# Optimization experiments

Hardware: AMD Instinct MI355X
Metric: run time of the kernel (lower is better)

## Reference

```python
import jax, jax.numpy as jnp
import numpy as np

B, S, DIN, DOUT = 4, 2048, 4096, 11008

def setup_inputs() -> dict:
    key = jax.random.key(0)
    k1, k2, k3 = jax.random.split(key, 3)
    x = jax.random.normal(k1, (B, S, DIN), dtype=jnp.float32)
    # int8 weight stored as int32 for portability; values in int8 range
    weight = jax.random.randint(k2, (DOUT, DIN), -127, 128, dtype=jnp.int32)
    scales = jax.random.uniform(k3, (DOUT,), dtype=jnp.float32) * 0.02 + 0.001
    return {"x": x, "weight": weight, "scales": scales}

def reference(x, weight, scales):
    # F.linear(input, weight.to(input.dtype)) * scales
    w = weight.astype(x.dtype)                      # [DOUT, DIN]
    out = jnp.einsum('bsi,oi->bso', x, w)           # [B, S, DOUT]
    return out * scales                             # per-out-channel scale
```

## Files before the change

### kernel.cpp

```cpp
#include <hip/hip_runtime.h>
#include <hip/hip_bf16.h>

#define M_DIM 8192
#define N_DIM 11008
#define K_DIM 4096

typedef __attribute__((ext_vector_type(8))) short bf16x8;
typedef __attribute__((ext_vector_type(4))) float f32x4;
typedef __attribute__((ext_vector_type(4))) int i32x4;

__device__ __forceinline__ short f2bf(float f) {
    __hip_bfloat16 h = __float2bfloat16(f);
    short s;
    __builtin_memcpy(&s, &h, sizeof(s));
    return s;
}

__device__ __forceinline__ void gload_lds16(const void* g, void* l) {
    __builtin_amdgcn_global_load_lds(
        (const __attribute__((address_space(1))) unsigned int*)g,
        (__attribute__((address_space(3))) unsigned int*)l, 16, 0, 0);
}

#define MFMAI8(A, Bv, C) __builtin_amdgcn_mfma_i32_16x16x64_i8((A), (Bv), (C), 0, 0, 0)
#define MFMA16(A, Bv, C) __builtin_amdgcn_mfma_f32_16x16x32_bf16((A), (Bv), (C), 0, 0, 0)


__global__ __launch_bounds__(256)
void quant_x_i8(const float* __restrict__ X, char* __restrict__ Xq,
                float* __restrict__ RS) {
    const int row  = blockIdx.x * 4 + (threadIdx.x >> 6);
    const int lane = threadIdx.x & 63;
    const float* xr = X + (size_t)row * K_DIM;

    float4 v[16];
    float am = 0.0f;
    #pragma unroll
    for (int c = 0; c < 16; ++c) {
        v[c] = *reinterpret_cast<const float4*>(xr + c * 256 + lane * 4);
        am = fmaxf(am, fmaxf(fmaxf(fabsf(v[c].x), fabsf(v[c].y)),
                             fmaxf(fabsf(v[c].z), fabsf(v[c].w))));
    }
    #pragma unroll
    for (int off = 1; off < 64; off <<= 1)
        am = fmaxf(am, __shfl_xor(am, off));

    const float inv = 127.0f / am;
    int* xq32 = reinterpret_cast<int*>(Xq + (size_t)row * K_DIM);
    #pragma unroll
    for (int c = 0; c < 16; ++c) {
        int c0 = __float2int_rn(v[c].x * inv);
        int c1 = __float2int_rn(v[c].y * inv);
        int c2 = __float2int_rn(v[c].z * inv);
        int c3 = __float2int_rn(v[c].w * inv);
        xq32[c * 64 + lane] = (c0 & 255) | ((c1 & 255) << 8) |
                              ((c2 & 255) << 16) | (c3 << 24);
    }
    if (lane == 0) RS[row] = am / 127.0f;
}


__global__ __launch_bounds__(256)
void cvt_w_i8(const int* __restrict__ W, char* __restrict__ Wq, int n16) {
    int i = blockIdx.x * blockDim.x + threadIdx.x;
    const int stride = gridDim.x * blockDim.x;
    for (; i < n16; i += stride) {
        const int4* p = reinterpret_cast<const int4*>(W + (size_t)i * 16);
        int4 a = p[0], b = p[1], c = p[2], d = p[3];
        int4 o;
        o.x = (a.x & 255) | ((a.y & 255) << 8) | ((a.z & 255) << 16) | (a.w << 24);
        o.y = (b.x & 255) | ((b.y & 255) << 8) | ((b.z & 255) << 16) | (b.w << 24);
        o.z = (c.x & 255) | ((c.y & 255) << 8) | ((c.z & 255) << 16) | (c.w << 24);
        o.w = (d.x & 255) | ((d.y & 255) << 8) | ((d.z & 255) << 16) | (d.w << 24);
        *reinterpret_cast<int4*>(Wq + (size_t)i * 16) = o;
    }
}


#define ST_A(T, DSTB) do { \
    const char* s_ = gA + (size_t)(T) * 128; \
    char* d_ = (DSTB) + aw; \
    gload_lds16(s_,                         d_); \
    gload_lds16(s_ + (size_t)64  * K_DIM,   d_ + 8192); \
    gload_lds16(s_ + (size_t)128 * K_DIM,   d_ + 16384); \
    gload_lds16(s_ + (size_t)192 * K_DIM,   d_ + 24576); \
} while (0)

#define ST_B(T, DSTB) do { \
    const char* s_ = gB + (size_t)(T) * 128; \
    char* d_ = (DSTB) + aw; \
    gload_lds16(s_,                         d_); \
    gload_lds16(s_ + (size_t)64  * K_DIM,   d_ + 8192); \
    gload_lds16(s_ + (size_t)128 * K_DIM,   d_ + 16384); \
    gload_lds16(s_ + (size_t)192 * K_DIM,   d_ + 24576); \
} while (0)

__global__ __launch_bounds__(512, 2)
void gemm_i8_nb(const char* __restrict__ Xq, const char* __restrict__ Wq,
                const float* __restrict__ RS, const float* __restrict__ SC,
                float* __restrict__ Out)
{
    __shared__ __attribute__((aligned(16))) char smem[163840];
    char* const As = smem;
    char* const Bs = smem + 65536;

    const int tid  = threadIdx.x;
    const int lane = tid & 63;
    const int w    = tid >> 6;
    const int wr   = w >> 2;
    const int wc   = w & 3;

    const int wg  = blockIdx.x;
    const int swz = (wg & 7) * 172 + (wg >> 3);
    const int by  = swz / 43;
    const int bx  = swz - by * 43;
    const int brow = by * 256;
    const int bcol = bx * 256;

    const int lr = lane >> 3;
    const int lc = (lane & 7) ^ lr;
    const char* gA = Xq + (size_t)(brow + w * 8 + lr) * K_DIM + (lc << 4);
    const char* gB = Wq + (size_t)(bcol + w * 8 + lr) * K_DIM + (lc << 4);
    const int aw = w * 1024;

    const int fa  = (wr * 128 + (lane & 15)) * 128;
    const int fb  = (wc * 64  + (lane & 15)) * 128;
    const int cs0 = (((lane >> 4) + 0) ^ (lane & 7)) * 16;
    const int cs1 = (((lane >> 4) + 4) ^ (lane & 7)) * 16;

    i32x4 acc[4][4] = {};
    i32x4 acc2[4][4] = {};

    char* Ac = As;            char* An = As + 32768;
    char* Bc = Bs;  char* B1 = Bs + 32768;  char* B2 = Bs + 65536;

    ST_B(0, Bc); ST_A(0, Ac);
    ST_B(1, B1);
    asm volatile("s_waitcnt vmcnt(4)" ::: "memory");
    __builtin_amdgcn_s_barrier();

    for (int t = 0; t < 32; ++t) {
        i32x4 a_[8][2], b_[4][2];
        #pragma unroll
        for (int m = 0; m < 4; ++m) {
            a_[m][0] = *(const i32x4*)(Ac + fa + m * 2048 + cs0);
            a_[m][1] = *(const i32x4*)(Ac + fa + m * 2048 + cs1);
        }
        #pragma unroll
        for (int n = 0; n < 4; ++n) {
            b_[n][0] = *(const i32x4*)(Bc + fb + n * 2048 + cs0);
            b_[n][1] = *(const i32x4*)(Bc + fb + n * 2048 + cs1);
        }
        if (t < 31) ST_A(t + 1, An);
        if (t < 30) ST_B(t + 2, B2);
        #pragma unroll
        for (int m = 0; m < 4; ++m) {
            a_[m + 4][0] = *(const i32x4*)(Ac + fa + (m + 4) * 2048 + cs0);
            a_[m + 4][1] = *(const i32x4*)(Ac + fa + (m + 4) * 2048 + cs1);
        }
        __builtin_amdgcn_s_setprio(1);
        #pragma unroll
        for (int m = 0; m < 4; ++m)
            #pragma unroll
            for (int n = 0; n < 4; ++n) {
                acc[m][n] = MFMAI8(a_[m][0], b_[n][0], acc[m][n]);
                acc[m][n] = MFMAI8(a_[m][1], b_[n][1], acc[m][n]);
            }
        #pragma unroll
        for (int m = 0; m < 4; ++m)
            #pragma unroll
            for (int n = 0; n < 4; ++n) {
                acc2[m][n] = MFMAI8(a_[m + 4][0], b_[n][0], acc2[m][n]);
                acc2[m][n] = MFMAI8(a_[m + 4][1], b_[n][1], acc2[m][n]);
            }
        __builtin_amdgcn_s_setprio(0);
        if (t < 31) {
            if (t < 30) asm volatile("s_waitcnt vmcnt(4)" ::: "memory");
            else        asm volatile("s_waitcnt vmcnt(0)" ::: "memory");
            __builtin_amdgcn_s_barrier();
        }
        char* tA = Ac; Ac = An; An = tA;
        char* tB = Bc; Bc = B1; B1 = B2; B2 = tB;
    }

    const int orow0 = brow + wr * 128 + ((lane >> 4) << 2);
    const int ocol0 = bcol + wc * 64 + (lane & 15);
    f32x4 rsv[8];
    #pragma unroll
    for (int m = 0; m < 8; ++m)
        rsv[m] = *reinterpret_cast<const f32x4*>(&RS[orow0 + m * 16]);
    #pragma unroll
    for (int n = 0; n < 4; ++n) {
        const float sc = SC[ocol0 + n * 16];
        #pragma unroll
        for (int m = 0; m < 4; ++m)
            #pragma unroll
            for (int j = 0; j < 4; ++j) {
                __builtin_nontemporal_store(
                    (float)acc[m][n][j] * (rsv[m][j] * sc),
                    &Out[(size_t)(orow0 + m * 16 + j) * N_DIM + (ocol0 + n * 16)]);
                __builtin_nontemporal_store(
                    (float)acc2[m][n][j] * (rsv[m + 4][j] * sc),
                    &Out[(size_t)(orow0 + (m + 4) * 16 + j) * N_DIM + (ocol0 + n * 16)]);
            }
    }
}


__global__ __launch_bounds__(256, 2)
void wo_int8_gemm_fused(const float* __restrict__ X, const int* __restrict__ W,
                        const float* __restrict__ SC, float* __restrict__ Out)
{
    __shared__ short Asf[128 * 64];
    __shared__ short Bsf[128 * 64];

    const int tid  = threadIdx.x;
    const int lane = tid & 63;
    const int wid  = tid >> 6;
    const int wrf  = wid >> 1;
    const int wcf  = wid & 1;
    const int brow = blockIdx.y * 128;
    const int bcol = blockIdx.x * 128;
    const int srow = tid >> 3;
    const int scol = (tid & 7) << 3;
    const int arow   = wrf * 64 + (lane & 15);
    const int brow_f = wcf * 64 + (lane & 15);
    const int koff   = (lane >> 4) << 3;

    f32x4 acc[4][4] = {};

    for (int k0 = 0; k0 < K_DIM; k0 += 64) {
        __syncthreads();
        #pragma unroll
        for (int p = 0; p < 4; ++p) {
            const int r = p * 32 + srow;
            const float4* xs = reinterpret_cast<const float4*>(
                X + (size_t)(brow + r) * K_DIM + (k0 + scol));
            float4 a0 = xs[0], a1 = xs[1];
            bf16x8 v;
            v[0] = f2bf(a0.x); v[1] = f2bf(a0.y); v[2] = f2bf(a0.z); v[3] = f2bf(a0.w);
            v[4] = f2bf(a1.x); v[5] = f2bf(a1.y); v[6] = f2bf(a1.z); v[7] = f2bf(a1.w);
            *reinterpret_cast<bf16x8*>(&Asf[(r * 64 + scol) ^ ((r & 7) << 3)]) = v;
        }
        #pragma unroll
        for (int p = 0; p < 4; ++p) {
            const int r = p * 32 + srow;
            const int4* ws = reinterpret_cast<const int4*>(
                W + (size_t)(bcol + r) * K_DIM + (k0 + scol));
            int4 b0 = ws[0], b1 = ws[1];
            bf16x8 v;
            v[0] = f2bf((float)b0.x); v[1] = f2bf((float)b0.y);
            v[2] = f2bf((float)b0.z); v[3] = f2bf((float)b0.w);
            v[4] = f2bf((float)b1.x); v[5] = f2bf((float)b1.y);
            v[6] = f2bf((float)b1.z); v[7] = f2bf((float)b1.w);
            *reinterpret_cast<bf16x8*>(&Bsf[(r * 64 + scol) ^ ((r & 7) << 3)]) = v;
        }
        __syncthreads();
        #pragma unroll
        for (int ks = 0; ks < 2; ++ks) {
            const int kb = ks * 32 + koff;
            bf16x8 af[4], bfr[4];
            #pragma unroll
            for (int m = 0; m < 4; ++m) {
                const int r = arow + m * 16;
                af[m] = *reinterpret_cast<const bf16x8*>(&Asf[(r * 64 + kb) ^ ((r & 7) << 3)]);
            }
            #pragma unroll
            for (int n = 0; n < 4; ++n) {
                const int r = brow_f + n * 16;
                bfr[n] = *reinterpret_cast<const bf16x8*>(&Bsf[(r * 64 + kb) ^ ((r & 7) << 3)]);
            }
            #pragma unroll
            for (int m = 0; m < 4; ++m)
                #pragma unroll
                for (int n = 0; n < 4; ++n)
                    acc[m][n] = MFMA16(af[m], bfr[n], acc[m][n]);
        }
    }

    const int orow0 = brow + wrf * 64 + ((lane >> 4) << 2);
    const int ocol0 = bcol + wcf * 64 + (lane & 15);
    #pragma unroll
    for (int n = 0; n < 4; ++n) {
        const float sc = SC[ocol0 + n * 16];
        #pragma unroll
        for (int m = 0; m < 4; ++m)
            #pragma unroll
            for (int j = 0; j < 4; ++j)
                Out[(size_t)(orow0 + m * 16 + j) * N_DIM + (ocol0 + n * 16)]
                    = acc[m][n][j] * sc;
    }
}

extern "C" void kernel_launch(void* const* d_in, const int* in_sizes, int n_in,
                              void* d_out, int out_size, void* d_ws, size_t ws_size,
                              hipStream_t stream) {
    const float* X  = (const float*)d_in[0];
    const int*   W  = (const int*)d_in[1];
    const float* SC = (const float*)d_in[2];
    float* Out = (float*)d_out;

    const size_t xq_bytes = (size_t)M_DIM * K_DIM;
    const size_t wq_bytes = (size_t)N_DIM * K_DIM;
    const size_t rs_bytes = (size_t)M_DIM * sizeof(float);
    if (ws_size >= xq_bytes + wq_bytes + rs_bytes) {
        char*  Xq = (char*)d_ws;
        char*  Wq = (char*)d_ws + xq_bytes;
        float* RS = (float*)((char*)d_ws + xq_bytes + wq_bytes);
        quant_x_i8<<<M_DIM / 4, 256, 0, stream>>>(X, Xq, RS);
        cvt_w_i8<<<2048, 256, 0, stream>>>(W, Wq, (int)((size_t)N_DIM * K_DIM / 16));
        gemm_i8_nb<<<(M_DIM / 256) * (N_DIM / 256), 512, 0, stream>>>(Xq, Wq, RS, SC, Out);
    } else {
        dim3 grid(N_DIM / 128, M_DIM / 128);
        wo_int8_gemm_fused<<<grid, 256, 0, stream>>>(X, W, SC, Out);
    }
}
```

Before: 453.9 us.

## Load GEMM fragments directly from global memory into registers, dropping LDS staging

Removes the shared-memory tiles, the async global-to-LDS copies, the multi-buffer rotation and the per-iteration barriers from the int8 GEMM. Each wave now loads its A and B MFMA fragments straight from global memory into registers every K step. This cuts LDS traffic and synchronisation, but gives up the data reuse across waves and the prefetch overlap. Global and L2 traffic goes up, and load latency is exposed with no software pipelining.

```diff
diff --git a/kernel.cpp b/kernel.cpp
--- a/kernel.cpp
+++ b/kernel.cpp
@@ -14,12 +14,6 @@
     short s;
     __builtin_memcpy(&s, &h, sizeof(s));
     return s;
-}
-
-__device__ __forceinline__ void gload_lds16(const void* g, void* l) {
-    __builtin_amdgcn_global_load_lds(
-        (const __attribute__((address_space(1))) unsigned int*)g,
-        (__attribute__((address_space(3))) unsigned int*)l, 16, 0, 0);
 }
 
 #define MFMAI8(A, Bv, C) __builtin_amdgcn_mfma_i32_16x16x64_i8((A), (Bv), (C), 0, 0, 0)
@@ -77,33 +71,11 @@
 }
 
 
-#define ST_A(T, DSTB) do { \
-    const char* s_ = gA + (size_t)(T) * 128; \
-    char* d_ = (DSTB) + aw; \
-    gload_lds16(s_,                         d_); \
-    gload_lds16(s_ + (size_t)64  * K_DIM,   d_ + 8192); \
-    gload_lds16(s_ + (size_t)128 * K_DIM,   d_ + 16384); \
-    gload_lds16(s_ + (size_t)192 * K_DIM,   d_ + 24576); \
-} while (0)
-
-#define ST_B(T, DSTB) do { \
-    const char* s_ = gB + (size_t)(T) * 128; \
-    char* d_ = (DSTB) + aw; \
-    gload_lds16(s_,                         d_); \
-    gload_lds16(s_ + (size_t)64  * K_DIM,   d_ + 8192); \
-    gload_lds16(s_ + (size_t)128 * K_DIM,   d_ + 16384); \
-    gload_lds16(s_ + (size_t)192 * K_DIM,   d_ + 24576); \
-} while (0)
-
 __global__ __launch_bounds__(512, 2)
-void gemm_i8_nb(const char* __restrict__ Xq, const char* __restrict__ Wq,
-                const float* __restrict__ RS, const float* __restrict__ SC,
-                float* __restrict__ Out)
+void gemm_i8_reg(const char* __restrict__ Xq, const char* __restrict__ Wq,
+                 const float* __restrict__ RS, const float* __restrict__ SC,
+                 float* __restrict__ Out)
 {
-    __shared__ __attribute__((aligned(16))) char smem[163840];
-    char* const As = smem;
-    char* const Bs = smem + 65536;
-
     const int tid  = threadIdx.x;
     const int lane = tid & 63;
     const int w    = tid >> 6;
@@ -117,70 +89,48 @@
     const int brow = by * 256;
     const int bcol = bx * 256;
 
-    const int lr = lane >> 3;
-    const int lc = (lane & 7) ^ lr;
-    const char* gA = Xq + (size_t)(brow + w * 8 + lr) * K_DIM + (lc << 4);
-    const char* gB = Wq + (size_t)(bcol + w * 8 + lr) * K_DIM + (lc << 4);
-    const int aw = w * 1024;
-
-    const int fa  = (wr * 128 + (lane & 15)) * 128;
-    const int fb  = (wc * 64  + (lane & 15)) * 128;
-    const int cs0 = (((lane >> 4) + 0) ^ (lane & 7)) * 16;
-    const int cs1 = (((lane >> 4) + 4) ^ (lane & 7)) * 16;
+    const char* pA = Xq + (size_t)(brow + wr * 128 + (lane & 15)) * K_DIM
+                        + ((lane >> 4) << 4);
+    const char* pB = Wq + (size_t)(bcol + wc * 64 + (lane & 15)) * K_DIM
+                        + ((lane >> 4) << 4);
 
     i32x4 acc[4][4] = {};
     i32x4 acc2[4][4] = {};
 
-    char* Ac = As;            char* An = As + 32768;
-    char* Bc = Bs;  char* B1 = Bs + 32768;  char* B2 = Bs + 65536;
-
-    ST_B(0, Bc); ST_A(0, Ac);
-    ST_B(1, B1);
-    asm volatile("s_waitcnt vmcnt(4)" ::: "memory");
-    __builtin_amdgcn_s_barrier();
-
     for (int t = 0; t < 32; ++t) {
-        i32x4 a_[8][2], b_[4][2];
+        const size_t ko = (size_t)t * 128;
+        i32x4 bf[4][2], af0[4][2], af1[4][2];
+        #pragma unroll
+        for (int n = 0; n < 4; ++n) {
+            bf[n][0] = *(const i32x4*)(pB + (size_t)n * 16 * K_DIM + ko);
+            bf[n][1] = *(const i32x4*)(pB + (size_t)n * 16 * K_DIM + ko + 64);
+        }
         #pragma unroll
         for (int m = 0; m < 4; ++m) {
-            a_[m][0] = *(const i32x4*)(Ac + fa + m * 2048 + cs0);
-            a_[m][1] = *(const i32x4*)(Ac + fa + m * 2048 + cs1);
-        }
-        #pragma unroll
-        for (int n = 0; n < 4; ++n) {
-            b_[n][0] = *(const i32x4*)(Bc + fb + n * 2048 + cs0);
-            b_[n][1] = *(const i32x4*)(Bc + fb + n * 2048 + cs1);
-        }
-        if (t < 31) ST_A(t + 1, An);
-        if (t < 30) ST_B(t + 2, B2);
+            af0[m][0] = *(const i32x4*)(pA + (size_t)m * 16 * K_DIM + ko);
+            af0[m][1] = *(const i32x4*)(pA + (size_t)m * 16 * K_DIM + ko + 64);
+        }
         #pragma unroll
         for (int m = 0; m < 4; ++m) {
-            a_[m + 4][0] = *(const i32x4*)(Ac + fa + (m + 4) * 2048 + cs0);
-            a_[m + 4][1] = *(const i32x4*)(Ac + fa + (m + 4) * 2048 + cs1);
+            af1[m][0] = *(const i32x4*)(pA + (size_t)(m + 4) * 16 * K_DIM + ko);
+            af1[m][1] = *(const i32x4*)(pA + (size_t)(m + 4) * 16 * K_DIM + ko + 64);
         }
         __builtin_amdgcn_s_setprio(1);
         #pragma unroll
         for (int m = 0; m < 4; ++m)
             #pragma unroll
             for (int n = 0; n < 4; ++n) {
-                acc[m][n] = MFMAI8(a_[m][0], b_[n][0], acc[m][n]);
-                acc[m][n] = MFMAI8(a_[m][1], b_[n][1], acc[m][n]);
+                acc[m][n] = MFMAI8(af0[m][0], bf[n][0], acc[m][n]);
+                acc[m][n] = MFMAI8(af0[m][1], bf[n][1], acc[m][n]);
             }
         #pragma unroll
         for (int m = 0; m < 4; ++m)
             #pragma unroll
             for (int n = 0; n < 4; ++n) {
-                acc2[m][n] = MFMAI8(a_[m + 4][0], b_[n][0], acc2[m][n]);
-                acc2[m][n] = MFMAI8(a_[m + 4][1], b_[n][1], acc2[m][n]);
+                acc2[m][n] = MFMAI8(af1[m][0], bf[n][0], acc2[m][n]);
+                acc2[m][n] = MFMAI8(af1[m][1], bf[n][1], acc2[m][n]);
             }
         __builtin_amdgcn_s_setprio(0);
-        if (t < 31) {
-            if (t < 30) asm volatile("s_waitcnt vmcnt(4)" ::: "memory");
-            else        asm volatile("s_waitcnt vmcnt(0)" ::: "memory");
-            __builtin_amdgcn_s_barrier();
-        }
-        char* tA = Ac; Ac = An; An = tA;
-        char* tB = Bc; Bc = B1; B1 = B2; B2 = tB;
     }
 
     const int orow0 = brow + wr * 128 + ((lane >> 4) << 2);
@@ -309,7 +259,7 @@
         float* RS = (float*)((char*)d_ws + xq_bytes + wq_bytes);
         quant_x_i8<<<M_DIM / 4, 256, 0, stream>>>(X, Xq, RS);
         cvt_w_i8<<<2048, 256, 0, stream>>>(W, Wq, (int)((size_t)N_DIM * K_DIM / 16));
-        gemm_i8_nb<<<(M_DIM / 256) * (N_DIM / 256), 512, 0, stream>>>(Xq, Wq, RS, SC, Out);
+        gemm_i8_reg<<<(M_DIM / 256) * (N_DIM / 256), 512, 0, stream>>>(Xq, Wq, RS, SC, Out);
     } else {
         dim3 grid(N_DIM / 128, M_DIM / 128);
         wo_int8_gemm_fused<<<grid, 256, 0, stream>>>(X, W, SC, Out);
```

Result: slower. 1.108 ms (+144.2%).
